# Optimization experiments

Measured on AMD Instinct MI355X. Metric: run time of the kernel, lower is better.

Reference implementation:

```python
import jax, jax.numpy as jnp
import numpy as np

N, IN_FEAT, OUT_FEAT, H = 4096, 256, 256, 8
D = OUT_FEAT // H  # per-head dim = 32
ADJ_DENSITY = 0.05


def setup_inputs() -> dict:
    key = jax.random.key(0)
    kx, kw, kb, ka, kadj = jax.random.split(key, 5)
    x = jax.random.normal(kx, (N, IN_FEAT), dtype=jnp.float32)
    # eqx.nn.Linear params: weight [out, in], bias [out]
    W = jax.random.normal(kw, (OUT_FEAT, IN_FEAT), dtype=jnp.float32) * (1.0 / np.sqrt(IN_FEAT))
    b = jax.random.normal(kb, (OUT_FEAT,), dtype=jnp.float32) * 0.01
    a = jax.random.normal(ka, (H, 2 * D), dtype=jnp.float32)
    adj_matrix = jax.random.bernoulli(kadj, ADJ_DENSITY, (N, N)).astype(jnp.float32)
    return {"x": x, "W": W, "b": b, "a": a, "adj_matrix": adj_matrix}


def reference(x, W, b, a, adj_matrix):
    num_nodes = x.shape[0]
    num_heads = a.shape[0]
    half = a.shape[1] // 2
    # projection: [N, H*D] -> [N, H, D]
    node_feats = (x @ W.T + b).reshape(num_nodes, num_heads, half)
    # per-head additive attention halves -> [N, H]
    logit_parent = (node_feats * a[None, :, :half]).sum(axis=-1)
    logit_child = (node_feats * a[None, :, half:]).sum(axis=-1)
    # [N, N, H] dense logits via broadcast-add
    attn_logits = logit_parent[:, None, :] + logit_child[None, :, :]
    attn_logits = jax.nn.leaky_relu(attn_logits, 0.2)
    # NOTE: faithful to source — masked entries set to 0.0 (not -inf)
    attn_logits = jnp.where(jnp.abs(adj_matrix)[..., None] != 0.0, attn_logits, 0.0)
    attn_probs = jax.nn.softmax(attn_logits, axis=1)
    out = jnp.einsum('ijh,jhc->ihc', attn_probs, node_feats)
    return out.reshape(num_nodes, -1)
```

## Files before the change

### kernel.cpp

```cpp
#include <hip/hip_runtime.h>

#define NN    4096
#define OF    256
#define NH    8
#define MAXNZ 384

typedef __attribute__((ext_vector_type(8))) short short8;
typedef __attribute__((ext_vector_type(4))) float f32x4;

__device__ __forceinline__ float bf2f(unsigned int u) {
    union { unsigned int i; float f; } v; v.i = u << 16; return v.f;
}
__device__ __forceinline__ unsigned short f2bf(float f) {
    union { float f; unsigned int i; } v; v.f = f;
    unsigned int x = v.i;
    return (unsigned short)((x + 0x7fffu + ((x >> 16) & 1u)) >> 16);
}
__device__ __forceinline__ unsigned int pk2bf(float a, float b) {
    return (unsigned int)f2bf(a) | ((unsigned int)f2bf(b) << 16);
}

__global__ __launch_bounds__(256) void k_pre(
    const float* __restrict__ adjf, const float* __restrict__ Wf,
    int* __restrict__ flag, unsigned short* __restrict__ Wbh,
    unsigned short* __restrict__ Wbl, float* __restrict__ zbase)
{
    __shared__ int viol;
    int t = threadIdx.x;
    int gid = blockIdx.x * 256 + t;
    if (t == 0) viol = 0;
    __syncthreads();
    int bad = 0;
    for (int k = t; k < NN; k += 256) {
        float v = adjf[k];
        if (!(v == 0.0f || v == 1.0f)) bad = 1;
    }
    if (bad) atomicAdd(&viol, 1);
    __syncthreads();
    int f = viol > 0;
    if (t == 0) *flag = f;

    zbase[gid] = 0.f;
    if (gid < 256) zbase[65536 + gid] = 0.f;
    if (!f) {
        float v = Wf[gid];
        unsigned short h = f2bf(v);
        Wbh[gid] = h; Wbl[gid] = f2bf(v - bf2f(h));
    }
}

__global__ __launch_bounds__(256) void k_proj(
    const void* __restrict__ xraw, const void* __restrict__ Wraw,
    const void* __restrict__ braw, const void* __restrict__ araw,
    const float* __restrict__ adjf, const int* __restrict__ flag,
    const unsigned short* __restrict__ Wbh, const unsigned short* __restrict__ Wbl,
    unsigned short* __restrict__ nfb, float* __restrict__ lp,
    float* __restrict__ lc, float* __restrict__ Stot,
    unsigned short* __restrict__ csr, int* __restrict__ nnz)
{
    __shared__ unsigned short xh[16][264], xl[16][264];

    int f = *flag;
    int t = threadIdx.x;
    int wave = t >> 6;
    int lane = t & 63;
    int tid  = blockIdx.x * 4 + wave;
    int mt = tid >> 4, nt = tid & 15;
    int lr = lane & 15;
    int kq = (lane >> 4) * 8;

    if (!f) {
        const float* xsrc = (const float*)xraw + (size_t)mt * 4096;
        #pragma unroll
        for (int q = 0; q < 16; q++) {
            int e = t + 256*q;
            float v = xsrc[e];
            unsigned short h = f2bf(v);
            xh[e >> 8][e & 255] = h;
            xl[e >> 8][e & 255] = f2bf(v - bf2f(h));
        }
        __syncthreads();
    }

    size_t wo = (size_t)(nt*16 + lr)*OF + kq;
    f32x4 acc = {0.f, 0.f, 0.f, 0.f};
    if (f) {
        const short8* xp = reinterpret_cast<const short8*>(
            (const unsigned short*)xraw + (size_t)(mt*16 + lr)*OF + kq);
        const short8* wp = reinterpret_cast<const short8*>(
            (const unsigned short*)Wraw + wo);
        #pragma unroll
        for (int kk = 0; kk < OF/32; kk++)
            acc = __builtin_amdgcn_mfma_f32_16x16x32_bf16(xp[kk*4], wp[kk*4], acc, 0, 0, 0);
    } else {
        const short8* wh = reinterpret_cast<const short8*>(Wbh + wo);
        const short8* wl = reinterpret_cast<const short8*>(Wbl + wo);
        #pragma unroll
        for (int kk = 0; kk < OF/32; kk++) {
            short8 ah = *reinterpret_cast<const short8*>(&xh[lr][kk*32 + kq]);
            short8 al = *reinterpret_cast<const short8*>(&xl[lr][kk*32 + kq]);
            short8 bh = wh[kk*4], bl = wl[kk*4];
            acc = __builtin_amdgcn_mfma_f32_16x16x32_bf16(ah, bh, acc, 0, 0, 0);
            acc = __builtin_amdgcn_mfma_f32_16x16x32_bf16(ah, bl, acc, 0, 0, 0);
            acc = __builtin_amdgcn_mfma_f32_16x16x32_bf16(al, bh, acc, 0, 0, 0);
        }
    }

    int col  = nt*16 + lr;
    int row0 = mt*16 + (lane >> 4) * 4;
    int h = col >> 5, cc = col & 31;
    float bias, apar, achd;
    if (f) {
        bias = bf2f((unsigned int)((const unsigned short*)braw)[col]);
        apar = bf2f((unsigned int)((const unsigned short*)araw)[h*64 + cc]);
        achd = bf2f((unsigned int)((const unsigned short*)araw)[h*64 + 32 + cc]);
    } else {
        bias = ((const float*)braw)[col];
        apar = ((const float*)araw)[h*64 + cc];
        achd = ((const float*)araw)[h*64 + 32 + cc];
    }
    float st = 0.f, pr[4], cr[4];
    #pragma unroll
    for (int r = 0; r < 4; r++) {
        float v = acc[r] + bias;
        nfb[(size_t)(row0 + r) * OF + col] = f2bf(v);
        st += v;
        pr[r] = v * apar;
        cr[r] = v * achd;
    }
    #pragma unroll
    for (int m = 1; m <= 8; m <<= 1) {
        #pragma unroll
        for (int r = 0; r < 4; r++) {
            pr[r] += __shfl_xor(pr[r], m, 64);
            cr[r] += __shfl_xor(cr[r], m, 64);
        }
    }
    if ((lane & 15) == 0) {
        #pragma unroll
        for (int r = 0; r < 4; r++) {
            atomicAdd(&lp[(row0 + r) * NH + h], pr[r]);
            atomicAdd(&lc[(row0 + r) * NH + h], cr[r]);
        }
    }
    st += __shfl_down(st, 16, 64);
    st += __shfl_down(st, 32, 64);
    if (lane < 16) atomicAdd(&Stot[col], st);

    int r = tid;
    unsigned long long m64 = 0ULL;
    if (f) {
        const uint4* arow = reinterpret_cast<const uint4*>(
            (const unsigned short*)adjf + (size_t)r * NN);
        #pragma unroll
        for (int g = 0; g < 8; g++) {
            uint4 v = arow[lane + 64*g];
            unsigned int wd[4] = {v.x, v.y, v.z, v.w};
            #pragma unroll
            for (int u = 0; u < 4; u++) {
                if (wd[u] & 0xffffu) m64 |= 1ULL << (g*8 + 2*u);
                if (wd[u] >> 16)     m64 |= 1ULL << (g*8 + 2*u + 1);
            }
        }
    } else {
        const uint4* arow = reinterpret_cast<const uint4*>(adjf + (size_t)r * NN);
        #pragma unroll 8
        for (int g = 0; g < 16; g++) {
            uint4 v = arow[lane + 64*g];
            if (v.x) m64 |= 1ULL << (g*4);
            if (v.y) m64 |= 1ULL << (g*4 + 1);
            if (v.z) m64 |= 1ULL << (g*4 + 2);
            if (v.w) m64 |= 1ULL << (g*4 + 3);
        }
    }
    int pc = __popcll(m64);
    int pref = pc;
    #pragma unroll
    for (int off = 1; off < 64; off <<= 1) {
        int u = __shfl_up(pref, off, 64);
        if (lane >= off) pref += u;
    }
    if (lane == 63) nnz[r] = min(pref, MAXNZ);
    {
        int pos = pref - pc;
        unsigned long long mm = m64;
        while (mm && pos < MAXNZ) {
            int q = __builtin_ctzll(mm);
            mm &= mm - 1;
            int j = f ? (lane*8 + ((q >> 3) << 9) + (q & 7))
                      : (lane*4 + ((q >> 2) << 8) + (q & 3));
            csr[(size_t)r * MAXNZ + pos++] = (unsigned short)j;
        }
    }
}

__global__ __launch_bounds__(256, 8) void k_attn(
    const int* __restrict__ flag, const unsigned short* __restrict__ csr,
    const int* __restrict__ nnz,
    const float* __restrict__ lp, const float* __restrict__ lc,
    const unsigned short* __restrict__ nfb, const float* __restrict__ Stot,
    void* __restrict__ outv)
{
    __shared__ float lps[NH];
    __shared__ int   jro[MAXNZ];
    __shared__ float wlist[MAXNZ][NH];
    __shared__ float zred[256];
    __shared__ float gred[3][256];

    int i = blockIdx.x;
    int t = threadIdx.x;
    int lane = t & 63, wid = t >> 6;
    int f = *flag;
    if (t < NH) lps[t] = lp[i*NH + t];
    int n = min(nnz[i], MAXNZ);

    if (t < MAXNZ/8) {
        uint4 v = reinterpret_cast<const uint4*>(csr + (size_t)i * MAXNZ)[t];
        unsigned int ws[4] = {v.x, v.y, v.z, v.w};
        #pragma unroll
        for (int u = 0; u < 4; u++) {
            jro[t*8 + 2*u]     = (int)(ws[u] & 0xffffu) * OF;
            jro[t*8 + 2*u + 1] = (int)(ws[u] >> 16) * OF;
        }
    }
    __syncthreads();

    int h8 = t & 7, c32 = t >> 3;
    float lph = lps[h8];
    float zp = 0.f;
    int k3 = c32;
    for (; k3 + 32 < n; k3 += 64) {
        int j0 = jro[k3] >> 5, j1 = jro[k3 + 32] >> 5;
        float l0 = lc[j0 + h8], l1 = lc[j1 + h8];
        float s0 = lph + l0; s0 = s0 > 0.f ? s0 : 0.2f * s0;
        float s1 = lph + l1; s1 = s1 > 0.f ? s1 : 0.2f * s1;
        float w0 = __expf(fminf(s0, 70.f)) - 1.f;
        float w1 = __expf(fminf(s1, 70.f)) - 1.f;
        wlist[k3][h8] = w0; wlist[k3 + 32][h8] = w1;
        zp += w0 + w1;
    }
    if (k3 < n) {
        float s = lph + lc[(jro[k3] >> 5) + h8];
        s = s > 0.f ? s : 0.2f * s;
        float w = __expf(fminf(s, 70.f)) - 1.f;
        wlist[k3][h8] = w;
        zp += w;
    }
    zred[t] = zp;
    __syncthreads();

    int hh = lane >> 3;
    int c4 = lane * 4;
    float a0 = 0.f, a1 = 0.f, a2 = 0.f, a3 = 0.f;
    int k = wid;
    for (; k + 28 < n; k += 32) {
        int jj[8]; float ww[8];
        #pragma unroll
        for (int u = 0; u < 8; u++) {
            jj[u] = __builtin_amdgcn_readfirstlane(jro[k + 4*u]);
            ww[u] = wlist[k + 4*u][hh];
        }
        uint2 d[8];
        #pragma unroll
        for (int u = 0; u < 8; u++)
            d[u] = *reinterpret_cast<const uint2*>(nfb + jj[u] + c4);
        #pragma unroll
        for (int u = 0; u < 8; u++) {
            a0 += ww[u] * bf2f(d[u].x & 0xffffu);
            a1 += ww[u] * bf2f(d[u].x >> 16);
            a2 += ww[u] * bf2f(d[u].y & 0xffffu);
            a3 += ww[u] * bf2f(d[u].y >> 16);
        }
    }
    for (; k < n; k += 4) {
        int j = __builtin_amdgcn_readfirstlane(jro[k]);
        float w = wlist[k][hh];
        uint2 d = *reinterpret_cast<const uint2*>(nfb + j + c4);
        a0 += w * bf2f(d.x & 0xffffu);
        a1 += w * bf2f(d.x >> 16);
        a2 += w * bf2f(d.y & 0xffffu);
        a3 += w * bf2f(d.y >> 16);
    }
    if (wid) {
        gred[wid-1][c4]   = a0; gred[wid-1][c4+1] = a1;
        gred[wid-1][c4+2] = a2; gred[wid-1][c4+3] = a3;
    }
    __syncthreads();

    if (wid == 0) {
        float z = zred[lane] + zred[lane+64] + zred[lane+128] + zred[lane+192];
        z += __shfl_down(z, 32, 64);
        z += __shfl_down(z, 16, 64);
        z += __shfl_down(z, 8, 64);
        float zfull = __shfl(z, hh, 64);
        float iz = 1.0f / (4096.0f + zfull);
        a0 += gred[0][c4]   + gred[1][c4]   + gred[2][c4];
        a1 += gred[0][c4+1] + gred[1][c4+1] + gred[2][c4+1];
        a2 += gred[0][c4+2] + gred[1][c4+2] + gred[2][c4+2];
        a3 += gred[0][c4+3] + gred[1][c4+3] + gred[2][c4+3];
        float4 stv = *reinterpret_cast<const float4*>(Stot + c4);
        float o0 = (stv.x + a0) * iz;
        float o1 = (stv.y + a1) * iz;
        float o2 = (stv.z + a2) * iz;
        float o3 = (stv.w + a3) * iz;
        if (f) {
            uint2 pk; pk.x = pk2bf(o0, o1); pk.y = pk2bf(o2, o3);
            *reinterpret_cast<uint2*>((unsigned short*)outv + (size_t)i*OF + c4) = pk;
        } else {
            float4 o = {o0, o1, o2, o3};
            *reinterpret_cast<float4*>((float*)outv + (size_t)i*OF + c4) = o;
        }
    }
}

extern "C" void kernel_launch(void* const* d_in, const int* in_sizes, int n_in,
                              void* d_out, int out_size, void* d_ws, size_t ws_size,
                              hipStream_t stream) {
    const void* x   = d_in[0];
    const void* W   = d_in[1];
    const void* b   = d_in[2];
    const void* a   = d_in[3];
    const void* adj = d_in[4];

    char* ws = (char*)d_ws;
    const size_t MB = 1024u*1024u, KB = 1024u;
    unsigned short* nfb  = (unsigned short*)(ws);
    float*          lp   = (float*)(ws + 2*MB);
    float*          lc   = (float*)(ws + 2*MB + 128*KB);
    float*          Stot = (float*)(ws + 2*MB + 256*KB);
    int*            flag = (int*)(ws + 2*MB + 257*KB);
    unsigned short* csr  = (unsigned short*)(ws + 2*MB + 258*KB);
    int*            nnz  = (int*)(ws + 5*MB + 258*KB);
    unsigned short* Wbh  = (unsigned short*)(ws + 6*MB);
    unsigned short* Wbl  = (unsigned short*)(ws + 6*MB + 128*KB);

    k_pre  <<<256,  256, 0, stream>>>((const float*)adj, (const float*)W,
                                      flag, Wbh, Wbl, lp);
    k_proj <<<1024, 256, 0, stream>>>(x, W, b, a, (const float*)adj, flag,
                                      Wbh, Wbl, nfb, lp, lc, Stot, csr, nnz);
    k_attn <<<NN,   256, 0, stream>>>(flag, csr, nnz, lp, lc, nfb, Stot, d_out);
}
```

Baseline: 159.1 us.

## Split projection and adjacency compaction into separate block roles within one kernel

The fused projection/CSR kernel now launches three times as many blocks. One in three blocks does the MFMA projection tile. The other two build CSR rows, with each row split across two waves that each cover half of the columns, and the halves are combined through a shared-memory prefix. This spreads the adjacency scan, which is bandwidth-bound, over more waves so it is no longer serialized behind the projection work in the same wave. The cost is more blocks and an extra block-level synchronization per CSR block.

```diff
diff --git a/kernel.cpp b/kernel.cpp
--- a/kernel.cpp
+++ b/kernel.cpp
@@ -49,7 +49,7 @@
     }
 }
 
-__global__ __launch_bounds__(256) void k_proj(
+__global__ __launch_bounds__(256) void k_main(
     const void* __restrict__ xraw, const void* __restrict__ Wraw,
     const void* __restrict__ braw, const void* __restrict__ araw,
     const float* __restrict__ adjf, const int* __restrict__ flag,
@@ -59,136 +59,152 @@
     unsigned short* __restrict__ csr, int* __restrict__ nnz)
 {
     __shared__ unsigned short xh[16][264], xl[16][264];
+    __shared__ int wtot[4];
 
     int f = *flag;
     int t = threadIdx.x;
     int wave = t >> 6;
     int lane = t & 63;
-    int tid  = blockIdx.x * 4 + wave;
-    int mt = tid >> 4, nt = tid & 15;
-    int lr = lane & 15;
-    int kq = (lane >> 4) * 8;
-
-    if (!f) {
-        const float* xsrc = (const float*)xraw + (size_t)mt * 4096;
-        #pragma unroll
-        for (int q = 0; q < 16; q++) {
-            int e = t + 256*q;
-            float v = xsrc[e];
-            unsigned short h = f2bf(v);
-            xh[e >> 8][e & 255] = h;
-            xl[e >> 8][e & 255] = f2bf(v - bf2f(h));
-        }
+    int bid = blockIdx.x;
+    int bdiv3 = bid / 3;
+
+    if (bid - bdiv3*3 == 0) {
+        int tid  = bdiv3 * 4 + wave;
+        int mt = tid >> 4, nt = tid & 15;
+        int lr = lane & 15;
+        int kq = (lane >> 4) * 8;
+
+        if (!f) {
+            const float* xsrc = (const float*)xraw + (size_t)mt * 4096;
+            #pragma unroll
+            for (int q = 0; q < 16; q++) {
+                int e = t + 256*q;
+                float v = xsrc[e];
+                unsigned short h = f2bf(v);
+                xh[e >> 8][e & 255] = h;
+                xl[e >> 8][e & 255] = f2bf(v - bf2f(h));
+            }
+            __syncthreads();
+        }
+
+        size_t wo = (size_t)(nt*16 + lr)*OF + kq;
+        f32x4 acc = {0.f, 0.f, 0.f, 0.f};
+        if (f) {
+            const short8* xp = reinterpret_cast<const short8*>(
+                (const unsigned short*)xraw + (size_t)(mt*16 + lr)*OF + kq);
+            const short8* wp = reinterpret_cast<const short8*>(
+                (const unsigned short*)Wraw + wo);
+            #pragma unroll
+            for (int kk = 0; kk < OF/32; kk++)
+                acc = __builtin_amdgcn_mfma_f32_16x16x32_bf16(xp[kk*4], wp[kk*4], acc, 0, 0, 0);
+        } else {
+            const short8* wh = reinterpret_cast<const short8*>(Wbh + wo);
+            const short8* wl = reinterpret_cast<const short8*>(Wbl + wo);
+            #pragma unroll
+            for (int kk = 0; kk < OF/32; kk++) {
+                short8 ah = *reinterpret_cast<const short8*>(&xh[lr][kk*32 + kq]);
+                short8 al = *reinterpret_cast<const short8*>(&xl[lr][kk*32 + kq]);
+                short8 bh = wh[kk*4], bl = wl[kk*4];
+                acc = __builtin_amdgcn_mfma_f32_16x16x32_bf16(ah, bh, acc, 0, 0, 0);
+                acc = __builtin_amdgcn_mfma_f32_16x16x32_bf16(ah, bl, acc, 0, 0, 0);
+                acc = __builtin_amdgcn_mfma_f32_16x16x32_bf16(al, bh, acc, 0, 0, 0);
+            }
+        }
+
+        int col  = nt*16 + lr;
+        int row0 = mt*16 + (lane >> 4) * 4;
+        int h = col >> 5, cc = col & 31;
+        float bias, apar, achd;
+        if (f) {
+            bias = bf2f((unsigned int)((const unsigned short*)braw)[col]);
+            apar = bf2f((unsigned int)((const unsigned short*)araw)[h*64 + cc]);
+            achd = bf2f((unsigned int)((const unsigned short*)araw)[h*64 + 32 + cc]);
+        } else {
+            bias = ((const float*)braw)[col];
+            apar = ((const float*)araw)[h*64 + cc];
+            achd = ((const float*)araw)[h*64 + 32 + cc];
+        }
+        float st = 0.f, pr[4], cr[4];
+        #pragma unroll
+        for (int r = 0; r < 4; r++) {
+            float v = acc[r] + bias;
+            nfb[(size_t)(row0 + r) * OF + col] = f2bf(v);
+            st += v;
+            pr[r] = v * apar;
+            cr[r] = v * achd;
+        }
+        #pragma unroll
+        for (int m = 1; m <= 8; m <<= 1) {
+            #pragma unroll
+            for (int r = 0; r < 4; r++) {
+                pr[r] += __shfl_xor(pr[r], m, 64);
+                cr[r] += __shfl_xor(cr[r], m, 64);
+            }
+        }
+        if ((lane & 15) == 0) {
+            #pragma unroll
+            for (int r = 0; r < 4; r++) {
+                atomicAdd(&lp[(row0 + r) * NH + h], pr[r]);
+                atomicAdd(&lc[(row0 + r) * NH + h], cr[r]);
+            }
+        }
+        st += __shfl_down(st, 16, 64);
+        st += __shfl_down(st, 32, 64);
+        if (lane < 16) atomicAdd(&Stot[col], st);
+    } else {
+        int sid = bid - bdiv3 - 1;
+        int r    = sid*2 + (wave >> 1);
+        int half = wave & 1;
+
+        unsigned int m32 = 0;
+        if (f) {
+            const uint4* ap = reinterpret_cast<const uint4*>(
+                (const unsigned short*)adjf + (size_t)r * NN + half * 2048);
+            #pragma unroll
+            for (int g = 0; g < 4; g++) {
+                uint4 v = ap[lane + 64*g];
+                unsigned int wd[4] = {v.x, v.y, v.z, v.w};
+                #pragma unroll
+                for (int u = 0; u < 4; u++) {
+                    if (wd[u] & 0xffffu) m32 |= 1u << (g*8 + 2*u);
+                    if (wd[u] >> 16)     m32 |= 1u << (g*8 + 2*u + 1);
+                }
+            }
+        } else {
+            const uint4* ap = reinterpret_cast<const uint4*>(
+                adjf + (size_t)r * NN + half * 2048);
+            #pragma unroll
+            for (int g = 0; g < 8; g++) {
+                uint4 v = ap[lane + 64*g];
+                if (v.x) m32 |= 1u << (g*4);
+                if (v.y) m32 |= 1u << (g*4 + 1);
+                if (v.z) m32 |= 1u << (g*4 + 2);
+                if (v.w) m32 |= 1u << (g*4 + 3);
+            }
+        }
+
+        int pc = __popc(m32);
+        int pref = pc;
+        #pragma unroll
+        for (int off = 1; off < 64; off <<= 1) {
+            int u = __shfl_up(pref, off, 64);
+            if (lane >= off) pref += u;
+        }
+        if (lane == 63) wtot[wave] = pref;
         __syncthreads();
-    }
-
-    size_t wo = (size_t)(nt*16 + lr)*OF + kq;
-    f32x4 acc = {0.f, 0.f, 0.f, 0.f};
-    if (f) {
-        const short8* xp = reinterpret_cast<const short8*>(
-            (const unsigned short*)xraw + (size_t)(mt*16 + lr)*OF + kq);
-        const short8* wp = reinterpret_cast<const short8*>(
-            (const unsigned short*)Wraw + wo);
-        #pragma unroll
-        for (int kk = 0; kk < OF/32; kk++)
-            acc = __builtin_amdgcn_mfma_f32_16x16x32_bf16(xp[kk*4], wp[kk*4], acc, 0, 0, 0);
-    } else {
-        const short8* wh = reinterpret_cast<const short8*>(Wbh + wo);
-        const short8* wl = reinterpret_cast<const short8*>(Wbl + wo);
-        #pragma unroll
-        for (int kk = 0; kk < OF/32; kk++) {
-            short8 ah = *reinterpret_cast<const short8*>(&xh[lr][kk*32 + kq]);
-            short8 al = *reinterpret_cast<const short8*>(&xl[lr][kk*32 + kq]);
-            short8 bh = wh[kk*4], bl = wl[kk*4];
-            acc = __builtin_amdgcn_mfma_f32_16x16x32_bf16(ah, bh, acc, 0, 0, 0);
-            acc = __builtin_amdgcn_mfma_f32_16x16x32_bf16(ah, bl, acc, 0, 0, 0);
-            acc = __builtin_amdgcn_mfma_f32_16x16x32_bf16(al, bh, acc, 0, 0, 0);
-        }
-    }
-
-    int col  = nt*16 + lr;
-    int row0 = mt*16 + (lane >> 4) * 4;
-    int h = col >> 5, cc = col & 31;
-    float bias, apar, achd;
-    if (f) {
-        bias = bf2f((unsigned int)((const unsigned short*)braw)[col]);
-        apar = bf2f((unsigned int)((const unsigned short*)araw)[h*64 + cc]);
-        achd = bf2f((unsigned int)((const unsigned short*)araw)[h*64 + 32 + cc]);
-    } else {
-        bias = ((const float*)braw)[col];
-        apar = ((const float*)araw)[h*64 + cc];
-        achd = ((const float*)araw)[h*64 + 32 + cc];
-    }
-    float st = 0.f, pr[4], cr[4];
-    #pragma unroll
-    for (int r = 0; r < 4; r++) {
-        float v = acc[r] + bias;
-        nfb[(size_t)(row0 + r) * OF + col] = f2bf(v);
-        st += v;
-        pr[r] = v * apar;
-        cr[r] = v * achd;
-    }
-    #pragma unroll
-    for (int m = 1; m <= 8; m <<= 1) {
-        #pragma unroll
-        for (int r = 0; r < 4; r++) {
-            pr[r] += __shfl_xor(pr[r], m, 64);
-            cr[r] += __shfl_xor(cr[r], m, 64);
-        }
-    }
-    if ((lane & 15) == 0) {
-        #pragma unroll
-        for (int r = 0; r < 4; r++) {
-            atomicAdd(&lp[(row0 + r) * NH + h], pr[r]);
-            atomicAdd(&lc[(row0 + r) * NH + h], cr[r]);
-        }
-    }
-    st += __shfl_down(st, 16, 64);
-    st += __shfl_down(st, 32, 64);
-    if (lane < 16) atomicAdd(&Stot[col], st);
-
-    int r = tid;
-    unsigned long long m64 = 0ULL;
-    if (f) {
-        const uint4* arow = reinterpret_cast<const uint4*>(
-            (const unsigned short*)adjf + (size_t)r * NN);
-        #pragma unroll
-        for (int g = 0; g < 8; g++) {
-            uint4 v = arow[lane + 64*g];
-            unsigned int wd[4] = {v.x, v.y, v.z, v.w};
-            #pragma unroll
-            for (int u = 0; u < 4; u++) {
-                if (wd[u] & 0xffffu) m64 |= 1ULL << (g*8 + 2*u);
-                if (wd[u] >> 16)     m64 |= 1ULL << (g*8 + 2*u + 1);
-            }
-        }
-    } else {
-        const uint4* arow = reinterpret_cast<const uint4*>(adjf + (size_t)r * NN);
-        #pragma unroll 8
-        for (int g = 0; g < 16; g++) {
-            uint4 v = arow[lane + 64*g];
-            if (v.x) m64 |= 1ULL << (g*4);
-            if (v.y) m64 |= 1ULL << (g*4 + 1);
-            if (v.z) m64 |= 1ULL << (g*4 + 2);
-            if (v.w) m64 |= 1ULL << (g*4 + 3);
-        }
-    }
-    int pc = __popcll(m64);
-    int pref = pc;
-    #pragma unroll
-    for (int off = 1; off < 64; off <<= 1) {
-        int u = __shfl_up(pref, off, 64);
-        if (lane >= off) pref += u;
-    }
-    if (lane == 63) nnz[r] = min(pref, MAXNZ);
-    {
-        int pos = pref - pc;
-        unsigned long long mm = m64;
+        int base = (wave == 1) ? wtot[0] : (wave == 3) ? wtot[2] : 0;
+        if (lane == 0) {
+            if (wave == 0) nnz[r] = min(wtot[0] + wtot[1], MAXNZ);
+            if (wave == 2) nnz[r] = min(wtot[2] + wtot[3], MAXNZ);
+        }
+        int pos = base + pref - pc;
+        unsigned int mm = m32;
+        int jb = half * 2048;
         while (mm && pos < MAXNZ) {
-            int q = __builtin_ctzll(mm);
+            int q = __builtin_ctz(mm);
             mm &= mm - 1;
-            int j = f ? (lane*8 + ((q >> 3) << 9) + (q & 7))
-                      : (lane*4 + ((q >> 2) << 8) + (q & 3));
+            int j = f ? (jb + lane*8 + ((q >> 3) << 9) + (q & 7))
+                      : (jb + lane*4 + ((q >> 2) << 8) + (q & 3));
             csr[(size_t)r * MAXNZ + pos++] = (unsigned short)j;
         }
     }
@@ -336,7 +352,7 @@
 
     k_pre  <<<256,  256, 0, stream>>>((const float*)adj, (const float*)W,
                                       flag, Wbh, Wbl, lp);
-    k_proj <<<1024, 256, 0, stream>>>(x, W, b, a, (const float*)adj, flag,
+    k_main <<<3072, 256, 0, stream>>>(x, W, b, a, (const float*)adj, flag,
                                       Wbh, Wbl, nfb, lp, lc, Stot, csr, nnz);
     k_attn <<<NN,   256, 0, stream>>>(flag, csr, nnz, lp, lc, nfb, Stot, d_out);
 }
```

Result: faster. 155.0 us (median of 2 runs) (-2.6%).
